# Kernel optimization log

Hardware: AMD Instinct MI355X
Metric: run time of the kernel (lower is better)

Reference implementation:

```python
import jax, jax.numpy as jnp
import numpy as np

B, T, C = 2, 2048, 1024
H = 16
HD = C // H  # head_dim = 64


def setup_inputs() -> dict:
    key = jax.random.key(0)
    ks = jax.random.split(key, 5)
    s = 0.02
    return {
        "x": jax.random.normal(ks[0], (B, T, C), dtype=jnp.float32),
        "Wqkv": jax.random.normal(ks[1], (C, 3 * C), dtype=jnp.float32) * s,
        "bqkv": jax.random.normal(ks[2], (3 * C,), dtype=jnp.float32) * s,
        "Wproj": jax.random.normal(ks[3], (C, C), dtype=jnp.float32) * s,
        "bproj": jax.random.normal(ks[4], (C,), dtype=jnp.float32) * s,
    }


def reference(x, Wqkv, bqkv, Wproj, bproj):
    b, t, c = x.shape
    qkv = x @ Wqkv + bqkv  # [B,T,3C]
    q, k, v = jnp.split(qkv, 3, axis=-1)
    # [B,T,C] -> [B,H,T,HD]
    q = q.reshape(b, t, H, HD).transpose(0, 2, 1, 3)
    k = k.reshape(b, t, H, HD).transpose(0, 2, 1, 3)
    v = v.reshape(b, t, H, HD).transpose(0, 2, 1, 3)
    scale = 1.0 / jnp.sqrt(jnp.float32(HD))
    att = jnp.einsum('bhqd,bhkd->bhqk', q, k) * scale  # [B,H,T,T]
    causal = jnp.tril(jnp.ones((t, t), dtype=bool))
    att = jnp.where(causal[None, None], att, jnp.float32(-jnp.inf))
    att = jax.nn.softmax(att, axis=-1)
    y = jnp.einsum('bhqk,bhkd->bhqd', att, v)  # [B,H,T,HD]
    y = y.transpose(0, 2, 1, 3).reshape(b, t, c)
    return y @ Wproj + bproj
```

## Files before the change

### kernel.cpp

```cpp
#include <hip/hip_runtime.h>

typedef unsigned short u16;
typedef __attribute__((ext_vector_type(4))) float f32x4;
typedef __attribute__((ext_vector_type(8))) short short8;

#define AS1 __attribute__((address_space(1)))
#define AS3 __attribute__((address_space(3)))

#define B_  2
#define T_  2048
#define C_  1024
#define H_  16
#define HD_ 64
#define N3C 3072
#define BT_ 4096

__device__ __forceinline__ u16 f2bf(float x) {
    unsigned u = __float_as_uint(x);
    u += 0x7fff + ((u >> 16) & 1);
    return (u16)(u >> 16);
}

__device__ __forceinline__ unsigned cvt_pk_bf16(float a, float b) {
    unsigned r;
    asm("v_cvt_pk_bf16_f32 %0, %1, %2" : "=v"(r) : "v"(a), "v"(b));
    return r;
}

__global__ __launch_bounds__(256)
void conv_all(const float* __restrict__ x, u16* __restrict__ xb,
              const float* __restrict__ Wq, u16* __restrict__ WqT,
              const float* __restrict__ Wp, u16* __restrict__ WpT) {
    __shared__ float tile[64][68];
    const int tid = threadIdx.x;
    const int b = blockIdx.x;
    if (b < 4096) {
        int i = b * 256 + tid;
        float4 f = ((const float4*)x)[i];
        uint2 o;
        o.x = cvt_pk_bf16(f.x, f.y);
        o.y = cvt_pk_bf16(f.z, f.w);
        ((uint2*)xb)[i] = o;
        return;
    }
    const float* W; u16* WT; int N, k0, n0;
    if (b < 4096 + 768) {
        int bb = b - 4096; W = Wq; WT = WqT; N = N3C;
        n0 = (bb % 48) * 64; k0 = (bb / 48) * 64;
    } else {
        int bb = b - 4864; W = Wp; WT = WpT; N = C_;
        n0 = (bb % 16) * 64; k0 = (bb / 16) * 64;
    }
    #pragma unroll
    for (int i = 0; i < 4; ++i) {
        int slot = tid + i * 256;
        int row = slot >> 4, c4 = (slot & 15) * 4;
        *(float4*)&tile[row][c4] = *(const float4*)&W[(size_t)(k0 + row) * N + n0 + c4];
    }
    __syncthreads();
    #pragma unroll
    for (int i = 0; i < 4; ++i) {
        int slot = tid + i * 256;
        int nn = slot >> 4, k4 = (slot & 15) * 4;
        uint2 o;
        o.x = cvt_pk_bf16(tile[k4 + 0][nn], tile[k4 + 1][nn]);
        o.y = cvt_pk_bf16(tile[k4 + 2][nn], tile[k4 + 3][nn]);
        *(uint2*)&WT[(size_t)(n0 + nn) * 1024 + k0 + k4] = o;
    }
}

__global__ __launch_bounds__(512, 2)
void qkv_gemm(const u16* __restrict__ A, const u16* __restrict__ BT,
              const float* __restrict__ bias,
              u16* __restrict__ q, u16* __restrict__ k, u16* __restrict__ vT) {
    __shared__ __align__(16) u16 As[2][256 * 64];
    __shared__ __align__(16) u16 Bs[2][192 * 64];
    const int tid  = threadIdx.x;
    const int lane = tid & 63, w = tid >> 6;
    const int wr = w >> 2, wc = w & 3;
    const int l15 = lane & 15, quad = lane >> 4;
    const int srow = lane >> 3, schunk = (lane & 7) ^ srow;

    const int bid = blockIdx.x;
    const int xcd = bid & 7, rr = bid >> 3;
    const int bm = (xcd << 1) | (rr & 1);
    const int bn = rr >> 1;
    const int m0 = bm * 256, n0 = bn * 192;

    const u16* gA = A  + (size_t)(m0 + w * 8  + srow) * 1024 + schunk * 8;
    const u16* gB = BT + (size_t)(n0 + w * 24 + srow) * 1024 + schunk * 8;

    auto stA = [&](int t, int qq) {
        __builtin_amdgcn_global_load_lds(
            (const AS1 void*)(gA + (size_t)qq * 64 * 1024 + t * 64),
            (AS3 void*)(&As[t & 1][(w * 8 + qq * 64) * 64]), 16, 0, 0);
    };
    auto stB = [&](int t, int g) {
        __builtin_amdgcn_global_load_lds(
            (const AS1 void*)(gB + (size_t)g * 8 * 1024 + t * 64),
            (AS3 void*)(&Bs[t & 1][(w * 24 + g * 8) * 64]), 16, 0, 0);
    };

    f32x4 acc[8][3] = {};

    stB(0, 0); stB(0, 1); stB(0, 2); stA(0, 0); stA(0, 2); stA(0, 1); stA(0, 3);
    asm volatile("s_waitcnt vmcnt(2)\n\ts_barrier" ::: "memory");

    #pragma unroll 1
    for (int t = 0; t < 16; ++t) {
        const u16* Ac = &As[t & 1][0];
        const u16* Bc = &Bs[t & 1][0];
        const bool st = (t < 15);
        short8 a[4], b[3];

        {
            const int xo = (quad ^ (l15 & 7)) * 8;
            #pragma unroll
            for (int mf = 0; mf < 4; ++mf)
                a[mf] = *(const short8*)&Ac[(wr * 128 + mf * 16 + l15) * 64 + xo];
            #pragma unroll
            for (int nf = 0; nf < 3; ++nf)
                b[nf] = *(const short8*)&Bc[(wc * 48 + nf * 16 + l15) * 64 + xo];
            if (st) { stB(t + 1, 0); stB(t + 1, 1); }
            asm volatile("s_barrier\n\ts_waitcnt lgkmcnt(0)" ::: "memory");
            __builtin_amdgcn_s_setprio(1);
            #pragma unroll
            for (int mf = 0; mf < 4; ++mf)
                #pragma unroll
                for (int nf = 0; nf < 3; ++nf)
                    acc[mf][nf] = __builtin_amdgcn_mfma_f32_16x16x32_bf16(a[mf], b[nf], acc[mf][nf], 0, 0, 0);
            __builtin_amdgcn_s_setprio(0);
            if (st) asm volatile("s_waitcnt vmcnt(2)\n\ts_barrier" ::: "memory");
            else    asm volatile("s_waitcnt vmcnt(0)\n\ts_barrier" ::: "memory");
        }
        {
            const int xo = (quad ^ (l15 & 7)) * 8;
            #pragma unroll
            for (int mf = 0; mf < 4; ++mf)
                a[mf] = *(const short8*)&Ac[(wr * 128 + (4 + mf) * 16 + l15) * 64 + xo];
            if (st) { stB(t + 1, 2); stA(t + 1, 0); }
            asm volatile("s_barrier\n\ts_waitcnt lgkmcnt(0)" ::: "memory");
            __builtin_amdgcn_s_setprio(1);
            #pragma unroll
            for (int mf = 0; mf < 4; ++mf)
                #pragma unroll
                for (int nf = 0; nf < 3; ++nf)
                    acc[4 + mf][nf] = __builtin_amdgcn_mfma_f32_16x16x32_bf16(a[mf], b[nf], acc[4 + mf][nf], 0, 0, 0);
            __builtin_amdgcn_s_setprio(0);
            asm volatile("s_barrier" ::: "memory");
        }
        {
            const int xo = ((4 + quad) ^ (l15 & 7)) * 8;
            #pragma unroll
            for (int mf = 0; mf < 4; ++mf)
                a[mf] = *(const short8*)&Ac[(wr * 128 + mf * 16 + l15) * 64 + xo];
            #pragma unroll
            for (int nf = 0; nf < 3; ++nf)
                b[nf] = *(const short8*)&Bc[(wc * 48 + nf * 16 + l15) * 64 + xo];
            if (st) stA(t + 1, 2);
            asm volatile("s_barrier\n\ts_waitcnt lgkmcnt(0)" ::: "memory");
            __builtin_amdgcn_s_setprio(1);
            #pragma unroll
            for (int mf = 0; mf < 4; ++mf)
                #pragma unroll
                for (int nf = 0; nf < 3; ++nf)
                    acc[mf][nf] = __builtin_amdgcn_mfma_f32_16x16x32_bf16(a[mf], b[nf], acc[mf][nf], 0, 0, 0);
            __builtin_amdgcn_s_setprio(0);
            asm volatile("s_barrier" ::: "memory");
        }
        {
            const int xo = ((4 + quad) ^ (l15 & 7)) * 8;
            #pragma unroll
            for (int mf = 0; mf < 4; ++mf)
                a[mf] = *(const short8*)&Ac[(wr * 128 + (4 + mf) * 16 + l15) * 64 + xo];
            if (st) { stA(t + 1, 1); stA(t + 1, 3); }
            asm volatile("s_barrier\n\ts_waitcnt lgkmcnt(0)" ::: "memory");
            __builtin_amdgcn_s_setprio(1);
            #pragma unroll
            for (int mf = 0; mf < 4; ++mf)
                #pragma unroll
                for (int nf = 0; nf < 3; ++nf)
                    acc[4 + mf][nf] = __builtin_amdgcn_mfma_f32_16x16x32_bf16(a[mf], b[nf], acc[4 + mf][nf], 0, 0, 0);
            __builtin_amdgcn_s_setprio(0);
            if (st) asm volatile("s_waitcnt vmcnt(2)\n\ts_barrier" ::: "memory");
            else    asm volatile("s_barrier" ::: "memory");
        }
    }

    const float QSCALE = 0.125f * 1.4426950408889634f;
    #pragma unroll
    for (int nf = 0; nf < 3; ++nf) {
        const int n = n0 + wc * 48 + nf * 16 + l15;
        const int which = n >> 10;
        const int nl = n & 1023, h = nl >> 6, d = nl & 63;
        const float bv = bias[n];
        #pragma unroll
        for (int mf = 0; mf < 8; ++mf) {
            const int mb = m0 + wr * 128 + mf * 16 + quad * 4;
            const int bb = mb >> 11, t0 = mb & 2047;
            f32x4 v4 = acc[mf][nf];
            if (which == 0) {
                size_t base = ((size_t)(bb * H_ + h) * T_ + t0) * HD_ + d;
                #pragma unroll
                for (int r = 0; r < 4; ++r)
                    q[base + (size_t)r * HD_] = f2bf((v4[r] + bv) * QSCALE);
            } else if (which == 1) {
                size_t base = ((size_t)(bb * H_ + h) * T_ + t0) * HD_ + d;
                #pragma unroll
                for (int r = 0; r < 4; ++r)
                    k[base + (size_t)r * HD_] = f2bf(v4[r] + bv);
            } else {
                uint2 o;
                o.x = cvt_pk_bf16(v4[0] + bv, v4[1] + bv);
                o.y = cvt_pk_bf16(v4[2] + bv, v4[3] + bv);
                *(uint2*)&vT[((size_t)(bb * H_ + h) * HD_ + d) * T_ + t0] = o;
            }
        }
    }
}

__global__ __launch_bounds__(256, 4)
void attn(const u16* __restrict__ q, const u16* __restrict__ k,
          const u16* __restrict__ vT, u16* __restrict__ y) {
    __shared__ __align__(16) u16 Ks[2 * 64 * 64];
    __shared__ __align__(16) u16 Vs[2 * 64 * 64];
    const int tid = threadIdx.x;
    const int lane = tid & 63, w = tid >> 6;
    const int l15 = lane & 15, quad = lane >> 4;
    const int srow = lane >> 3, schunk = (lane & 7) ^ srow;
    const int idx = blockIdx.x;
    const int bh = idx & 31;
    const int qt = 31 - (idx >> 5);
    const u16* qp = q  + (size_t)bh * T_ * HD_;
    const u16* kp = k  + (size_t)bh * T_ * HD_;
    const u16* vp = vT + (size_t)bh * HD_ * T_;

    const int qrow = qt * 64 + w * 16 + l15;
    short8 qf[2];
    #pragma unroll
    for (int s = 0; s < 2; ++s)
        qf[s] = *(const short8*)&qp[(size_t)qrow * HD_ + s * 32 + quad * 8];

    auto stage = [&](int buf, int kt) {
        const int kb = kt * 64;
        asm volatile("s_waitcnt lgkmcnt(0)" ::: "memory");
        #pragma unroll
        for (int j = 0; j < 2; ++j) {
            int row = w * 16 + j * 8 + srow;
            __builtin_amdgcn_global_load_lds(
                (const AS1 void*)(kp + (size_t)(kb + row) * HD_ + schunk * 8),
                (AS3 void*)(Ks + buf * (64 * 64) + (w * 16 + j * 8) * 64), 16, 0, 0);
            __builtin_amdgcn_global_load_lds(
                (const AS1 void*)(vp + (size_t)row * T_ + kb + schunk * 8),
                (AS3 void*)(Vs + buf * (64 * 64) + (w * 16 + j * 8) * 64), 16, 0, 0);
        }
    };

    f32x4 o[4] = {};
    float l = 0.f;
    stage(0, 0);

    for (int kt = 0; kt <= qt; ++kt) {
        const int kb = kt * 64;
        const int cur = kt & 1;
        if (kt < qt) {
            stage(cur ^ 1, kt + 1);
            asm volatile("s_waitcnt vmcnt(4)\n\ts_barrier" ::: "memory");
        } else {
            asm volatile("s_waitcnt vmcnt(0)\n\ts_barrier" ::: "memory");
        }
        u16* Kc = Ks + cur * (64 * 64);
        const u16* Vc = Vs + cur * (64 * 64);

        short8 ka[4][2], va[4][2];
        #pragma unroll
        for (int ct = 0; ct < 4; ++ct)
            #pragma unroll
            for (int s = 0; s < 2; ++s) {
                int xo = ((s * 4 + quad) ^ (l15 & 7)) * 8;
                ka[ct][s] = *(const short8*)&Kc[(ct * 16 + l15) * 64 + xo];
                va[ct][s] = *(const short8*)&Vc[(ct * 16 + l15) * 64 + xo];
            }
        asm volatile("s_waitcnt lgkmcnt(0)\n\ts_barrier" ::: "memory");

        f32x4 st[4] = {};
        #pragma unroll
        for (int s = 0; s < 2; ++s)
            #pragma unroll
            for (int ct = 0; ct < 4; ++ct)
                st[ct] = __builtin_amdgcn_mfma_f32_16x16x32_bf16(ka[ct][s], qf[s], st[ct], 0, 0, 0);

        float pe[16];
        #pragma unroll
        for (int ct = 0; ct < 4; ++ct)
            #pragma unroll
            for (int r = 0; r < 4; ++r)
                pe[ct * 4 + r] = exp2f(st[ct][r]);
        if (kt == qt) {
            #pragma unroll
            for (int ct = 0; ct < 4; ++ct)
                #pragma unroll
                for (int r = 0; r < 4; ++r)
                    if ((kb + ct * 16 + quad * 4 + r) > qrow) pe[ct * 4 + r] = 0.f;
        }
        float psum = 0.f;
        #pragma unroll
        for (int i = 0; i < 16; ++i) psum += pe[i];
        l += psum;

        u16* Pw = Kc + (w * 16 + l15) * 64;
        #pragma unroll
        for (int ct = 0; ct < 4; ++ct) {
            int chunk = ct * 2 + (quad >> 1);
            int off = ((chunk ^ (l15 & 7)) << 3) + (quad & 1) * 4;
            uint2 pk;
            pk.x = cvt_pk_bf16(pe[ct * 4 + 0], pe[ct * 4 + 1]);
            pk.y = cvt_pk_bf16(pe[ct * 4 + 2], pe[ct * 4 + 3]);
            *(uint2*)&Pw[off] = pk;
        }
        asm volatile("s_waitcnt lgkmcnt(0)" ::: "memory");

        #pragma unroll
        for (int s = 0; s < 2; ++s) {
            short8 pb = *(const short8*)&Pw[(((s * 4 + quad) ^ (l15 & 7)) << 3)];
            #pragma unroll
            for (int n = 0; n < 4; ++n)
                o[n] = __builtin_amdgcn_mfma_f32_16x16x32_bf16(va[n][s], pb, o[n], 0, 0, 0);
        }
    }

    l += __shfl_xor(l, 16); l += __shfl_xor(l, 32);
    const float inv = 1.f / l;
    const int bb = bh >> 4, h = bh & 15;
    #pragma unroll
    for (int n = 0; n < 4; ++n) {
        uint2 pk;
        pk.x = cvt_pk_bf16(o[n][0] * inv, o[n][1] * inv);
        pk.y = cvt_pk_bf16(o[n][2] * inv, o[n][3] * inv);
        *(uint2*)&y[((size_t)(bb * T_ + qrow)) * C_ + h * 64 + n * 16 + quad * 4] = pk;
    }
}

__global__ __launch_bounds__(256, 3)
void proj_gemm(const u16* __restrict__ A, const u16* __restrict__ BT,
               const float* __restrict__ bias, float* __restrict__ out) {
    __shared__ __align__(16) u16 As[2 * 128 * 64];
    __shared__ __align__(16) u16 Bs[2 * 64 * 64];
    const int m0 = blockIdx.y * 128, n0 = blockIdx.x * 64;
    const int tid = threadIdx.x;
    const int lane = tid & 63, w = tid >> 6;
    const int l15 = lane & 15, quad = lane >> 4;
    const int row0 = (w & 1) * 64, col0 = (w >> 1) * 32;
    const int srow = lane >> 3;
    const int schunk = (lane & 7) ^ srow;
    f32x4 acc[4][2] = {};

    auto stage = [&](int buf, int k0) {
        #pragma unroll
        for (int j = 0; j < 4; ++j) {
            int rbase = w * 32 + j * 8;
            const u16* ga = A + (size_t)(m0 + rbase + srow) * 1024 + k0 + schunk * 8;
            __builtin_amdgcn_global_load_lds((const AS1 void*)ga,
                (AS3 void*)(As + buf * (128 * 64) + rbase * 64), 16, 0, 0);
        }
        #pragma unroll
        for (int j = 0; j < 2; ++j) {
            int rbase = w * 16 + j * 8;
            const u16* gb = BT + (size_t)(n0 + rbase + srow) * 1024 + k0 + schunk * 8;
            __builtin_amdgcn_global_load_lds((const AS1 void*)gb,
                (AS3 void*)(Bs + buf * (64 * 64) + rbase * 64), 16, 0, 0);
        }
    };

    stage(0, 0);
    #pragma unroll
    for (int it = 0; it < 16; ++it) {
        const int cur = it & 1;
        if (it + 1 < 16) {
            stage(cur ^ 1, (it + 1) * 64);
            asm volatile("s_waitcnt vmcnt(6)\n\ts_barrier" ::: "memory");
        } else {
            asm volatile("s_waitcnt vmcnt(0)\n\ts_barrier" ::: "memory");
        }
        const u16* Ac = As + cur * (128 * 64);
        const u16* Bc = Bs + cur * (64 * 64);
        #pragma unroll
        for (int s = 0; s < 2; ++s) {
            short8 a[4], b[2];
            #pragma unroll
            for (int rt = 0; rt < 4; ++rt) {
                int row = row0 + rt * 16 + l15;
                a[rt] = *(const short8*)&Ac[row * 64 + (((s * 4 + quad) ^ (l15 & 7)) * 8)];
            }
            #pragma unroll
            for (int ct = 0; ct < 2; ++ct) {
                int row = col0 + ct * 16 + l15;
                b[ct] = *(const short8*)&Bc[row * 64 + (((s * 4 + quad) ^ (l15 & 7)) * 8)];
            }
            #pragma unroll
            for (int rt = 0; rt < 4; ++rt)
                #pragma unroll
                for (int ct = 0; ct < 2; ++ct)
                    acc[rt][ct] = __builtin_amdgcn_mfma_f32_16x16x32_bf16(a[rt], b[ct], acc[rt][ct], 0, 0, 0);
        }
        asm volatile("s_waitcnt lgkmcnt(0)\n\ts_barrier" ::: "memory");
    }

    #pragma unroll
    for (int ct = 0; ct < 2; ++ct) {
        int n = n0 + col0 + ct * 16 + l15;
        float bv = bias[n];
        #pragma unroll
        for (int rt = 0; rt < 4; ++rt) {
            int mb = m0 + row0 + rt * 16 + quad * 4;
            f32x4 v4 = acc[rt][ct];
            #pragma unroll
            for (int r = 0; r < 4; ++r)
                out[(size_t)(mb + r) * 1024 + n] = v4[r] + bv;
        }
    }
}

extern "C" void kernel_launch(void* const* d_in, const int* in_sizes, int n_in,
                              void* d_out, int out_size, void* d_ws, size_t ws_size,
                              hipStream_t stream) {
    const float* x     = (const float*)d_in[0];
    const float* Wqkv  = (const float*)d_in[1];
    const float* bqkv  = (const float*)d_in[2];
    const float* Wproj = (const float*)d_in[3];
    const float* bproj = (const float*)d_in[4];

    u16* xb     = (u16*)d_ws;
    u16* WqkvT  = xb + (size_t)4 * 1024 * 1024;
    u16* WprojT = WqkvT + (size_t)3 * 1024 * 1024;
    u16* q      = WprojT + (size_t)1024 * 1024;
    u16* kk     = q + (size_t)4 * 1024 * 1024;
    u16* vT     = kk + (size_t)4 * 1024 * 1024;
    u16* y      = vT + (size_t)4 * 1024 * 1024;

    conv_all<<<5120, 256, 0, stream>>>(x, xb, Wqkv, WqkvT, Wproj, WprojT);
    qkv_gemm<<<256, 512, 0, stream>>>(xb, WqkvT, bqkv, q, kk, vT);
    attn<<<1024, 256, 0, stream>>>(q, kk, vT, y);
    proj_gemm<<<dim3(C_ / 64, BT_ / 128), 256, 0, stream>>>(y, WprojT, bproj, (float*)d_out);
}
```

Baseline: 173.7 us.

## Split attention warps across key halves and query pairs, reducing partials via LDS

The attention kernel changes its warp decomposition. Each warp previously owned 16 query rows across all 64 keys of a tile. Now each warp handles 32 query rows against half of the key tile, so every K/V fragment loaded from LDS feeds two query groups, which cuts LDS reads per MFMA. The price is a dedicated P buffer in shared memory, more accumulator registers, and a final cross-warp reduction of output and row-sum partials through LDS with extra barriers.

Result: slower. 177.9 us (+2.4%).

```diff
diff --git a/kernel.cpp b/kernel.cpp
--- a/kernel.cpp
+++ b/kernel.cpp
@@ -224,8 +224,10 @@
           const u16* __restrict__ vT, u16* __restrict__ y) {
     __shared__ __align__(16) u16 Ks[2 * 64 * 64];
     __shared__ __align__(16) u16 Vs[2 * 64 * 64];
+    __shared__ __align__(16) u16 Ps[64 * 64];
     const int tid = threadIdx.x;
     const int lane = tid & 63, w = tid >> 6;
+    const int kh = w >> 1, qh = w & 1;
     const int l15 = lane & 15, quad = lane >> 4;
     const int srow = lane >> 3, schunk = (lane & 7) ^ srow;
     const int idx = blockIdx.x;
@@ -235,11 +237,14 @@
     const u16* kp = k  + (size_t)bh * T_ * HD_;
     const u16* vp = vT + (size_t)bh * HD_ * T_;
 
-    const int qrow = qt * 64 + w * 16 + l15;
-    short8 qf[2];
-    #pragma unroll
-    for (int s = 0; s < 2; ++s)
-        qf[s] = *(const short8*)&qp[(size_t)qrow * HD_ + s * 32 + quad * 8];
+    short8 qf[2][2];
+    #pragma unroll
+    for (int qg = 0; qg < 2; ++qg) {
+        const int qrow = qt * 64 + qh * 32 + qg * 16 + l15;
+        #pragma unroll
+        for (int s = 0; s < 2; ++s)
+            qf[qg][s] = *(const short8*)&qp[(size_t)qrow * HD_ + s * 32 + quad * 8];
+    }
 
     auto stage = [&](int buf, int kt) {
         const int kb = kt * 64;
@@ -256,12 +261,11 @@
         }
     };
 
-    f32x4 o[4] = {};
-    float l = 0.f;
+    f32x4 o[4][2] = {};
+    float l[2] = {0.f, 0.f};
     stage(0, 0);
 
     for (int kt = 0; kt <= qt; ++kt) {
-        const int kb = kt * 64;
         const int cur = kt & 1;
         if (kt < qt) {
             stage(cur ^ 1, kt + 1);
@@ -269,75 +273,114 @@
         } else {
             asm volatile("s_waitcnt vmcnt(0)\n\ts_barrier" ::: "memory");
         }
-        u16* Kc = Ks + cur * (64 * 64);
+        const u16* Kc = Ks + cur * (64 * 64);
         const u16* Vc = Vs + cur * (64 * 64);
 
-        short8 ka[4][2], va[4][2];
-        #pragma unroll
-        for (int ct = 0; ct < 4; ++ct)
-            #pragma unroll
-            for (int s = 0; s < 2; ++s) {
-                int xo = ((s * 4 + quad) ^ (l15 & 7)) * 8;
-                ka[ct][s] = *(const short8*)&Kc[(ct * 16 + l15) * 64 + xo];
-                va[ct][s] = *(const short8*)&Vc[(ct * 16 + l15) * 64 + xo];
+        short8 ka[2][2], va[4];
+        #pragma unroll
+        for (int t = 0; t < 2; ++t)
+            #pragma unroll
+            for (int s = 0; s < 2; ++s)
+                ka[t][s] = *(const short8*)&Kc[(kh * 32 + t * 16 + l15) * 64 + (((s * 4 + quad) ^ (l15 & 7)) * 8)];
+        #pragma unroll
+        for (int n = 0; n < 4; ++n)
+            va[n] = *(const short8*)&Vc[(n * 16 + l15) * 64 + (((kh * 4 + quad) ^ (l15 & 7)) * 8)];
+        asm volatile("s_waitcnt lgkmcnt(0)\n\ts_barrier" ::: "memory");
+
+        f32x4 st[2][2] = {};
+        #pragma unroll
+        for (int s = 0; s < 2; ++s)
+            #pragma unroll
+            for (int t = 0; t < 2; ++t)
+                #pragma unroll
+                for (int qg = 0; qg < 2; ++qg)
+                    st[t][qg] = __builtin_amdgcn_mfma_f32_16x16x32_bf16(ka[t][s], qf[qg][s], st[t][qg], 0, 0, 0);
+
+        float pe[2][2][4];
+        #pragma unroll
+        for (int t = 0; t < 2; ++t)
+            #pragma unroll
+            for (int qg = 0; qg < 2; ++qg)
+                #pragma unroll
+                for (int r = 0; r < 4; ++r)
+                    pe[t][qg][r] = exp2f(st[t][qg][r]);
+        if (kt == qt) {
+            #pragma unroll
+            for (int t = 0; t < 2; ++t)
+                #pragma unroll
+                for (int qg = 0; qg < 2; ++qg)
+                    #pragma unroll
+                    for (int r = 0; r < 4; ++r)
+                        if ((kh * 32 + t * 16 + quad * 4 + r) > (qh * 32 + qg * 16 + l15))
+                            pe[t][qg][r] = 0.f;
+        }
+        #pragma unroll
+        for (int qg = 0; qg < 2; ++qg) {
+            float ps = 0.f;
+            #pragma unroll
+            for (int t = 0; t < 2; ++t)
+                #pragma unroll
+                for (int r = 0; r < 4; ++r)
+                    ps += pe[t][qg][r];
+            l[qg] += ps;
+        }
+
+        #pragma unroll
+        for (int t = 0; t < 2; ++t)
+            #pragma unroll
+            for (int qg = 0; qg < 2; ++qg) {
+                int off = (((kh * 4 + t * 2 + (quad >> 1)) ^ (l15 & 7)) << 3) + (quad & 1) * 4;
+                uint2 pk;
+                pk.x = cvt_pk_bf16(pe[t][qg][0], pe[t][qg][1]);
+                pk.y = cvt_pk_bf16(pe[t][qg][2], pe[t][qg][3]);
+                *(uint2*)&Ps[(qh * 32 + qg * 16 + l15) * 64 + off] = pk;
             }
-        asm volatile("s_waitcnt lgkmcnt(0)\n\ts_barrier" ::: "memory");
-
-        f32x4 st[4] = {};
-        #pragma unroll
-        for (int s = 0; s < 2; ++s)
-            #pragma unroll
-            for (int ct = 0; ct < 4; ++ct)
-                st[ct] = __builtin_amdgcn_mfma_f32_16x16x32_bf16(ka[ct][s], qf[s], st[ct], 0, 0, 0);
-
-        float pe[16];
-        #pragma unroll
-        for (int ct = 0; ct < 4; ++ct)
-            #pragma unroll
-            for (int r = 0; r < 4; ++r)
-                pe[ct * 4 + r] = exp2f(st[ct][r]);
-        if (kt == qt) {
-            #pragma unroll
-            for (int ct = 0; ct < 4; ++ct)
-                #pragma unroll
-                for (int r = 0; r < 4; ++r)
-                    if ((kb + ct * 16 + quad * 4 + r) > qrow) pe[ct * 4 + r] = 0.f;
-        }
-        float psum = 0.f;
-        #pragma unroll
-        for (int i = 0; i < 16; ++i) psum += pe[i];
-        l += psum;
-
-        u16* Pw = Kc + (w * 16 + l15) * 64;
-        #pragma unroll
-        for (int ct = 0; ct < 4; ++ct) {
-            int chunk = ct * 2 + (quad >> 1);
-            int off = ((chunk ^ (l15 & 7)) << 3) + (quad & 1) * 4;
-            uint2 pk;
-            pk.x = cvt_pk_bf16(pe[ct * 4 + 0], pe[ct * 4 + 1]);
-            pk.y = cvt_pk_bf16(pe[ct * 4 + 2], pe[ct * 4 + 3]);
-            *(uint2*)&Pw[off] = pk;
-        }
         asm volatile("s_waitcnt lgkmcnt(0)" ::: "memory");
 
         #pragma unroll
-        for (int s = 0; s < 2; ++s) {
-            short8 pb = *(const short8*)&Pw[(((s * 4 + quad) ^ (l15 & 7)) << 3)];
+        for (int qg = 0; qg < 2; ++qg) {
+            short8 pb = *(const short8*)&Ps[(qh * 32 + qg * 16 + l15) * 64 + (((kh * 4 + quad) ^ (l15 & 7)) << 3)];
             #pragma unroll
             for (int n = 0; n < 4; ++n)
-                o[n] = __builtin_amdgcn_mfma_f32_16x16x32_bf16(va[n][s], pb, o[n], 0, 0, 0);
-        }
-    }
-
-    l += __shfl_xor(l, 16); l += __shfl_xor(l, 32);
-    const float inv = 1.f / l;
-    const int bb = bh >> 4, h = bh & 15;
-    #pragma unroll
-    for (int n = 0; n < 4; ++n) {
-        uint2 pk;
-        pk.x = cvt_pk_bf16(o[n][0] * inv, o[n][1] * inv);
-        pk.y = cvt_pk_bf16(o[n][2] * inv, o[n][3] * inv);
-        *(uint2*)&y[((size_t)(bb * T_ + qrow)) * C_ + h * 64 + n * 16 + quad * 4] = pk;
+                o[n][qg] = __builtin_amdgcn_mfma_f32_16x16x32_bf16(va[n], pb, o[n][qg], 0, 0, 0);
+        }
+    }
+
+    l[0] += __shfl_xor(l[0], 16); l[0] += __shfl_xor(l[0], 32);
+    l[1] += __shfl_xor(l[1], 16); l[1] += __shfl_xor(l[1], 32);
+
+    float* ob = (float*)Vs;
+    float* lb = (float*)Ps;
+    asm volatile("s_waitcnt lgkmcnt(0)\n\ts_barrier" ::: "memory");
+    if (kh == 1) {
+        const int base = (qh * 64 + lane) * 32;
+        #pragma unroll
+        for (int n = 0; n < 4; ++n)
+            #pragma unroll
+            for (int qg = 0; qg < 2; ++qg)
+                *(f32x4*)&ob[base + (n * 2 + qg) * 4] = o[n][qg];
+        lb[(qh * 64 + lane) * 2 + 0] = l[0];
+        lb[(qh * 64 + lane) * 2 + 1] = l[1];
+    }
+    asm volatile("s_waitcnt lgkmcnt(0)\n\ts_barrier" ::: "memory");
+    if (kh == 0) {
+        const int base = (qh * 64 + lane) * 32;
+        float linv[2];
+        linv[0] = 1.f / (l[0] + lb[(qh * 64 + lane) * 2 + 0]);
+        linv[1] = 1.f / (l[1] + lb[(qh * 64 + lane) * 2 + 1]);
+        const int bb = bh >> 4, h = bh & 15;
+        #pragma unroll
+        for (int qg = 0; qg < 2; ++qg) {
+            const int qrow = qt * 64 + qh * 32 + qg * 16 + l15;
+            #pragma unroll
+            for (int n = 0; n < 4; ++n) {
+                f32x4 ov = o[n][qg] + *(const f32x4*)&ob[base + (n * 2 + qg) * 4];
+                uint2 pk;
+                pk.x = cvt_pk_bf16(ov[0] * linv[qg], ov[1] * linv[qg]);
+                pk.y = cvt_pk_bf16(ov[2] * linv[qg], ov[3] * linv[qg]);
+                *(uint2*)&y[((size_t)(bb * T_ + qrow)) * C_ + h * 64 + n * 16 + quad * 4] = pk;
+            }
+        }
     }
 }
 
@@ -395,7 +438,7 @@
             #pragma unroll
             for (int ct = 0; ct < 2; ++ct) {
                 int row = col0 + ct * 16 + l15;
-                b[ct] = *(const short8*)&Bc[row * 64 + (((s * 4 + quad) ^ (l15 & 7)) * 8)];
+                b[ct] = *(const short8*)&Bs[cur * (64 * 64) + row * 64 + (((s * 4 + quad) ^ (l15 & 7)) * 8)];
             }
             #pragma unroll
             for (int rt = 0; rt < 4; ++rt)
```

## Replace LDS round-trip for P with ds_bpermute and restructure K/V prefetch barriers

Applied to the files above, without the earlier changes.

The softmax probabilities are now redistributed across lanes with ds_bpermute shuffles, replacing the write-to-LDS/read-back through the K buffer. This frees the K buffer, so the second barrier per tile is removed and the next tile's prefetch is issued after the current tile's K/V fragments are loaded into registers rather than before. The aim is fewer barriers and LDS stores per iteration. In exchange, each iteration now waits on vmcnt(0), so there is less load/compute overlap, and it adds 16 bpermute ops per iteration.

Result: no change. 173.8 us (+0.1%).

```diff
diff --git a/kernel.cpp b/kernel.cpp
--- a/kernel.cpp
+++ b/kernel.cpp
@@ -3,6 +3,7 @@
 typedef unsigned short u16;
 typedef __attribute__((ext_vector_type(4))) float f32x4;
 typedef __attribute__((ext_vector_type(8))) short short8;
+typedef __attribute__((ext_vector_type(4))) int i32x4;
 
 #define AS1 __attribute__((address_space(1)))
 #define AS3 __attribute__((address_space(3)))
@@ -243,7 +244,6 @@
 
     auto stage = [&](int buf, int kt) {
         const int kb = kt * 64;
-        asm volatile("s_waitcnt lgkmcnt(0)" ::: "memory");
         #pragma unroll
         for (int j = 0; j < 2; ++j) {
             int row = w * 16 + j * 8 + srow;
@@ -260,16 +260,15 @@
     float l = 0.f;
     stage(0, 0);
 
+    const int a0 = (l15 + ((quad & 1) << 5)) << 2;
+    const int a1 = a0 + 64;
+    const bool hiq = (quad >> 1) != 0;
+
     for (int kt = 0; kt <= qt; ++kt) {
         const int kb = kt * 64;
         const int cur = kt & 1;
-        if (kt < qt) {
-            stage(cur ^ 1, kt + 1);
-            asm volatile("s_waitcnt vmcnt(4)\n\ts_barrier" ::: "memory");
-        } else {
-            asm volatile("s_waitcnt vmcnt(0)\n\ts_barrier" ::: "memory");
-        }
-        u16* Kc = Ks + cur * (64 * 64);
+        asm volatile("s_waitcnt vmcnt(0)\n\ts_barrier" ::: "memory");
+        const u16* Kc = Ks + cur * (64 * 64);
         const u16* Vc = Vs + cur * (64 * 64);
 
         short8 ka[4][2], va[4][2];
@@ -281,7 +280,7 @@
                 ka[ct][s] = *(const short8*)&Kc[(ct * 16 + l15) * 64 + xo];
                 va[ct][s] = *(const short8*)&Vc[(ct * 16 + l15) * 64 + xo];
             }
-        asm volatile("s_waitcnt lgkmcnt(0)\n\ts_barrier" ::: "memory");
+        if (kt < qt) stage(cur ^ 1, kt + 1);
 
         f32x4 st[4] = {};
         #pragma unroll
@@ -308,21 +307,29 @@
         for (int i = 0; i < 16; ++i) psum += pe[i];
         l += psum;
 
-        u16* Pw = Kc + (w * 16 + l15) * 64;
+        int pk[4][2];
         #pragma unroll
         for (int ct = 0; ct < 4; ++ct) {
-            int chunk = ct * 2 + (quad >> 1);
-            int off = ((chunk ^ (l15 & 7)) << 3) + (quad & 1) * 4;
-            uint2 pk;
-            pk.x = cvt_pk_bf16(pe[ct * 4 + 0], pe[ct * 4 + 1]);
-            pk.y = cvt_pk_bf16(pe[ct * 4 + 2], pe[ct * 4 + 3]);
-            *(uint2*)&Pw[off] = pk;
-        }
-        asm volatile("s_waitcnt lgkmcnt(0)" ::: "memory");
+            pk[ct][0] = (int)cvt_pk_bf16(pe[ct * 4 + 0], pe[ct * 4 + 1]);
+            pk[ct][1] = (int)cvt_pk_bf16(pe[ct * 4 + 2], pe[ct * 4 + 3]);
+        }
 
         #pragma unroll
         for (int s = 0; s < 2; ++s) {
-            short8 pb = *(const short8*)&Pw[(((s * 4 + quad) ^ (l15 & 7)) << 3)];
+            int e0 = __builtin_amdgcn_ds_bpermute(a0, pk[2 * s + 0][0]);
+            int g0 = __builtin_amdgcn_ds_bpermute(a0, pk[2 * s + 1][0]);
+            int e1 = __builtin_amdgcn_ds_bpermute(a0, pk[2 * s + 0][1]);
+            int g1 = __builtin_amdgcn_ds_bpermute(a0, pk[2 * s + 1][1]);
+            int e2 = __builtin_amdgcn_ds_bpermute(a1, pk[2 * s + 0][0]);
+            int g2 = __builtin_amdgcn_ds_bpermute(a1, pk[2 * s + 1][0]);
+            int e3 = __builtin_amdgcn_ds_bpermute(a1, pk[2 * s + 0][1]);
+            int g3 = __builtin_amdgcn_ds_bpermute(a1, pk[2 * s + 1][1]);
+            i32x4 pbi;
+            pbi[0] = hiq ? g0 : e0;
+            pbi[1] = hiq ? g1 : e1;
+            pbi[2] = hiq ? g2 : e2;
+            pbi[3] = hiq ? g3 : e3;
+            short8 pb = __builtin_bit_cast(short8, pbi);
             #pragma unroll
             for (int n = 0; n < 4; ++n)
                 o[n] = __builtin_amdgcn_mfma_f32_16x16x32_bf16(va[n][s], pb, o[n], 0, 0, 0);
```
